# Optimization experiments

Measured on AMD Instinct MI355X. Metric: run time of the kernel, lower is better.

## Reference

```python
import jax, jax.numpy as jnp
import numpy as np

BATCH = 65536
IN_DIM = 512
LATENT = 32
NUM_TRIL = LATENT * (LATENT + 1) // 2  # 528
# torch.tril_indices returns row-major order, same as np.tril_indices
_ROWS, _COLS = np.tril_indices(LATENT)
ROWS = jnp.asarray(_ROWS)
COLS = jnp.asarray(_COLS)
BN_EPS = 1e-5
LRELU_SLOPE = 0.01


def setup_inputs() -> dict:
    key = jax.random.key(0)
    ks = jax.random.split(key, 12)
    x = jax.random.normal(ks[0], (BATCH, IN_DIM), dtype=jnp.float32)
    s_enc = 1.0 / np.sqrt(IN_DIM)
    s_lat = 1.0 / np.sqrt(LATENT)
    return {
        "x": x,
        "W_enc": jax.random.uniform(ks[1], (IN_DIM, LATENT), minval=-s_enc, maxval=s_enc, dtype=jnp.float32),
        "b_enc": jax.random.uniform(ks[2], (LATENT,), minval=-s_enc, maxval=s_enc, dtype=jnp.float32),
        "bn_gamma": jnp.ones((LATENT,), dtype=jnp.float32),
        "bn_beta": jnp.zeros((LATENT,), dtype=jnp.float32),
        "bn_mean": 0.1 * jax.random.normal(ks[3], (LATENT,), dtype=jnp.float32),
        "bn_var": jax.random.uniform(ks[4], (LATENT,), minval=0.5, maxval=1.5, dtype=jnp.float32),
        "W_mu": jax.random.uniform(ks[5], (LATENT, LATENT), minval=-s_lat, maxval=s_lat, dtype=jnp.float32),
        "b_mu": jax.random.uniform(ks[6], (LATENT,), minval=-s_lat, maxval=s_lat, dtype=jnp.float32),
        "W_ch": jax.random.uniform(ks[7], (LATENT, NUM_TRIL), minval=-s_lat, maxval=s_lat, dtype=jnp.float32),
        "b_ch": jax.random.uniform(ks[8], (NUM_TRIL,), minval=-s_lat, maxval=s_lat, dtype=jnp.float32),
    }


def _leaky_relu(v):
    return jnp.where(v >= 0, v, LRELU_SLOPE * v)


def reference(x, W_enc, b_enc, bn_gamma, bn_beta, bn_mean, bn_var, W_mu, b_mu, W_ch, b_ch):
    # downsampled_enc: Linear(512, latent) -> BatchNorm1d (eval mode) -> LeakyReLU
    h = x @ W_enc + b_enc                                        # [B, L]
    h = bn_gamma * (h - bn_mean) * jax.lax.rsqrt(bn_var + BN_EPS) + bn_beta
    h = _leaky_relu(h)
    # mu head
    mus = _leaky_relu(h @ W_mu + b_mu)                           # [B, L]
    # log-cholesky head -> 528 lower-triangular elements
    elts = _leaky_relu(h @ W_ch + b_ch)                          # [B, 528]
    B = x.shape[0]
    L = jnp.zeros((B, LATENT, LATENT), dtype=jnp.float32)
    L = L.at[:, ROWS, COLS].set(elts)                            # scatter into lower triangle
    di = jnp.arange(LATENT)
    diag = L[:, di, di]
    diag = jnp.clip(jax.nn.softplus(diag), 0.001, 100.0) + 0.01
    L = L.at[:, di, di].set(diag)
    # cov = L L^T + 0.01 I
    cov = jnp.einsum('bij,bkj->bik', L, L) + 0.01 * jnp.eye(LATENT, dtype=jnp.float32)
    return (h, mus, cov)
```

## Files before the change

### kernel.cpp

```cpp
#include <hip/hip_runtime.h>
#include <math.h>

constexpr int BATCH  = 65536;
constexpr int IN_DIM = 512;
constexpr int LATENT = 32;
constexpr int NTRIL  = 528;
constexpr float BN_EPS = 1e-5f;
constexpr float SLOPE  = 0.01f;

constexpr int RPB  = 64;
constexpr int SUBR = 16;
constexpr int HSTR = 36;
constexpr int PSTR = 36;

constexpr int LSTRIDE = 584;

__device__ __host__ __forceinline__ constexpr int rstart(int i) {
    const int g = i >> 2, r = i & 3;
    return 4 * (i + 2 * g * (g - 1) + r * g);
}

__device__ __forceinline__ float leaky(float v) {
    return v >= 0.0f ? v : SLOPE * v;
}

extern "C" __global__ __launch_bounds__(256, 4)
void enc_kernel(const float* __restrict__ x,
                const float* __restrict__ W_enc,
                const float* __restrict__ b_enc,
                const float* __restrict__ bn_gamma,
                const float* __restrict__ bn_beta,
                const float* __restrict__ bn_mean,
                const float* __restrict__ bn_var,
                float* __restrict__ h_out)
{
    __shared__ float part[4][RPB][PSTR];

    const int t = threadIdx.x;
    const int w = __builtin_amdgcn_readfirstlane(t >> 6);
    const int l = t & 63;
    const int row0 = blockIdx.x * RPB;

    {
        const float4* __restrict__ xp =
            (const float4*)(x + (size_t)(row0 + l) * IN_DIM + w * (IN_DIM / 4));
        const float* __restrict__ Wq = W_enc + (w * (IN_DIM / 4)) * LATENT;

        float acc[LATENT];
        #pragma unroll
        for (int c = 0; c < LATENT; ++c) acc[c] = 0.0f;

        float4 q0 = xp[0];
        float4 q1 = xp[1];
        #pragma unroll 2
        for (int k4 = 0; k4 < IN_DIM / 16; ++k4) {
            const float4 xv = q0;
            q0 = q1;
            const int pf = (k4 < IN_DIM / 16 - 2) ? (k4 + 2) : (IN_DIM / 16 - 1);
            q1 = xp[pf];

            const float* __restrict__ Wk = Wq + (4 * k4) * LATENT;
            #pragma unroll
            for (int c = 0; c < LATENT; ++c) acc[c] = fmaf(xv.x, Wk[c],            acc[c]);
            #pragma unroll
            for (int c = 0; c < LATENT; ++c) acc[c] = fmaf(xv.y, Wk[LATENT + c],   acc[c]);
            #pragma unroll
            for (int c = 0; c < LATENT; ++c) acc[c] = fmaf(xv.z, Wk[2*LATENT + c], acc[c]);
            #pragma unroll
            for (int c = 0; c < LATENT; ++c) acc[c] = fmaf(xv.w, Wk[3*LATENT + c], acc[c]);
        }

        #pragma unroll
        for (int c4 = 0; c4 < LATENT / 4; ++c4)
            *(float4*)&part[w][l][4 * c4] =
                make_float4(acc[4*c4+0], acc[4*c4+1], acc[4*c4+2], acc[4*c4+3]);
    }
    __syncthreads();

    {
        const int r  = t >> 2;
        const int c0 = (t & 3) * 8;
        float v[8];
        #pragma unroll
        for (int i = 0; i < 8; ++i) v[i] = 0.0f;
        #pragma unroll
        for (int ww = 0; ww < 4; ++ww) {
            const float4 p0 = *(const float4*)&part[ww][r][c0];
            const float4 p1 = *(const float4*)&part[ww][r][c0 + 4];
            v[0]+=p0.x; v[1]+=p0.y; v[2]+=p0.z; v[3]+=p0.w;
            v[4]+=p1.x; v[5]+=p1.y; v[6]+=p1.z; v[7]+=p1.w;
        }
        float hv[8];
        #pragma unroll
        for (int i = 0; i < 8; ++i) {
            const int c = c0 + i;
            float u = v[i] + b_enc[c];
            u = bn_gamma[c] * (u - bn_mean[c]) * rsqrtf(bn_var[c] + BN_EPS) + bn_beta[c];
            hv[i] = leaky(u);
        }
        float4* __restrict__ hp = (float4*)(h_out + (size_t)(row0 + r) * LATENT + c0);
        hp[0] = make_float4(hv[0], hv[1], hv[2], hv[3]);
        hp[1] = make_float4(hv[4], hv[5], hv[6], hv[7]);
    }
}

extern "C" __global__ __launch_bounds__(256)
void dec_kernel(const float* __restrict__ h_in,
                const float* __restrict__ W_mu,
                const float* __restrict__ b_mu,
                const float* __restrict__ W_ch,
                const float* __restrict__ b_ch,
                float* __restrict__ mu_out,
                float* __restrict__ cov_out)
{
    __shared__ float h_sh[RPB][HSTR];
    __shared__ float L_sh[SUBR * LSTRIDE];

    const int t = threadIdx.x;
    const int row0 = blockIdx.x * RPB;

    {
        float4* z4 = (float4*)L_sh;
        const float4 z = make_float4(0.f, 0.f, 0.f, 0.f);
        #pragma unroll 1
        for (int s = t; s < SUBR * LSTRIDE / 4; s += 256) z4[s] = z;
    }

    {
        const int r  = t >> 2;
        const int c0 = (t & 3) * 8;
        const float4* __restrict__ hg =
            (const float4*)(h_in + (size_t)(row0 + r) * LATENT + c0);
        const float4 a0 = hg[0];
        const float4 a1 = hg[1];
        *(float4*)&h_sh[r][c0]     = a0;
        *(float4*)&h_sh[r][c0 + 4] = a1;
    }
    __syncthreads();

    {
        const int c = t & 31;
        const int g = t >> 5;
        float wmu[LATENT];
        #pragma unroll
        for (int k = 0; k < LATENT; ++k) wmu[k] = W_mu[k * LATENT + c];
        const float bm = b_mu[c];
        #pragma unroll
        for (int j = 0; j < 8; ++j) {
            const int r = g * 8 + j;
            const float4* __restrict__ hr = (const float4*)&h_sh[r][0];
            float a = bm;
            #pragma unroll
            for (int k4 = 0; k4 < 8; ++k4) {
                const float4 hvv = hr[k4];
                a += hvv.x*wmu[4*k4+0] + hvv.y*wmu[4*k4+1]
                   + hvv.z*wmu[4*k4+2] + hvv.w*wmu[4*k4+3];
            }
            mu_out[(size_t)(row0 + r) * LATENT + c] = leaky(a);
        }
    }

    #pragma unroll 1
    for (int sb = 0; sb < RPB / SUBR; ++sb) {
        const int rbl = sb * SUBR;

        #pragma unroll 1
        for (int jid = t; jid < 132 * 8; jid += 256) {
            const int q  = jid % 132;
            const int rg = jid / 132;
            const int j0 = 4 * q;
            const int r0s = rbl + rg * 2;

            float4 a0 = make_float4(b_ch[j0+0], b_ch[j0+1], b_ch[j0+2], b_ch[j0+3]);
            float4 a1 = a0;

            const float* __restrict__ wbase = W_ch + j0;
            #pragma unroll
            for (int kq = 0; kq < 8; ++kq) {
                const float4 w0 = *(const float4*)(wbase + (4*kq + 0) * NTRIL);
                const float4 w1 = *(const float4*)(wbase + (4*kq + 1) * NTRIL);
                const float4 w2 = *(const float4*)(wbase + (4*kq + 2) * NTRIL);
                const float4 w3 = *(const float4*)(wbase + (4*kq + 3) * NTRIL);
                const float4 h0 = *(const float4*)&h_sh[r0s    ][4*kq];
                const float4 h1 = *(const float4*)&h_sh[r0s + 1][4*kq];
                a0.x += h0.x*w0.x + h0.y*w1.x + h0.z*w2.x + h0.w*w3.x;
                a0.y += h0.x*w0.y + h0.y*w1.y + h0.z*w2.y + h0.w*w3.y;
                a0.z += h0.x*w0.z + h0.y*w1.z + h0.z*w2.z + h0.w*w3.z;
                a0.w += h0.x*w0.w + h0.y*w1.w + h0.z*w2.w + h0.w*w3.w;
                a1.x += h1.x*w0.x + h1.y*w1.x + h1.z*w2.x + h1.w*w3.x;
                a1.y += h1.x*w0.y + h1.y*w1.y + h1.z*w2.y + h1.w*w3.y;
                a1.z += h1.x*w0.z + h1.y*w1.z + h1.z*w2.z + h1.w*w3.z;
                a1.w += h1.x*w0.w + h1.y*w1.w + h1.z*w2.w + h1.w*w3.w;
            }

            #pragma unroll
            for (int e = 0; e < 4; ++e) {
                const int j = j0 + e;
                int ri = (int)((sqrtf(8.0f * (float)j + 1.0f) - 1.0f) * 0.5f);
                if ((ri + 1) * (ri + 2) / 2 <= j) ++ri;
                if (ri * (ri + 1) / 2 > j) --ri;
                const int ci = j - ri * (ri + 1) / 2;
                const bool isdiag = (ci == ri);
                const int off = rstart(ri) + ci;

                float v0 = (e == 0) ? a0.x : (e == 1) ? a0.y : (e == 2) ? a0.z : a0.w;
                float v1 = (e == 0) ? a1.x : (e == 1) ? a1.y : (e == 2) ? a1.z : a1.w;
                v0 = leaky(v0);
                v1 = leaky(v1);
                if (isdiag) {
                    float s0 = v0 > 20.0f ? v0 : log1pf(__expf(v0));
                    float s1 = v1 > 20.0f ? v1 : log1pf(__expf(v1));
                    v0 = fminf(fmaxf(s0, 0.001f), 100.0f) + 0.01f;
                    v1 = fminf(fmaxf(s1, 0.001f), 100.0f) + 0.01f;
                }
                L_sh[(r0s - rbl) * LSTRIDE + off]       = v0;
                L_sh[(r0s - rbl + 1) * LSTRIDE + off]   = v1;
            }
        }
        __syncthreads();

        {
            const int lr = t >> 4;
            const int p  = t & 15;
            const float* __restrict__ Lb = L_sh + lr * LSTRIDE;

            float a0[16];
            {
                const int s0 = rstart(p);
                #pragma unroll
                for (int qq = 0; qq < 4; ++qq) {
                    const float4 v = *(const float4*)(Lb + s0 + 4*qq);
                    a0[4*qq+0] = (4*qq+0 <= p) ? v.x : 0.0f;
                    a0[4*qq+1] = (4*qq+1 <= p) ? v.y : 0.0f;
                    a0[4*qq+2] = (4*qq+2 <= p) ? v.z : 0.0f;
                    a0[4*qq+3] = (4*qq+3 <= p) ? v.w : 0.0f;
                }
            }
            float a1[32];
            {
                const int i1 = p + 16;
                const int s1 = rstart(i1);
                #pragma unroll
                for (int qq = 0; qq < 8; ++qq) {
                    const float4 v = *(const float4*)(Lb + s1 + 4*qq);
                    a1[4*qq+0] = (4*qq+0 <= i1) ? v.x : 0.0f;
                    a1[4*qq+1] = (4*qq+1 <= i1) ? v.y : 0.0f;
                    a1[4*qq+2] = (4*qq+2 <= i1) ? v.z : 0.0f;
                    a1[4*qq+3] = (4*qq+3 <= i1) ? v.w : 0.0f;
                }
            }

            const size_t grow = (size_t)(row0 + rbl + lr);
            float* __restrict__ cov0 =
                cov_out + grow * (size_t)(LATENT * LATENT) + (size_t)p * LATENT;
            float* __restrict__ cov1 = cov0 + 16 * LATENT;

            float c0[4], c1[4];
            #pragma unroll
            for (int k = 0; k < LATENT; ++k) {
                const int qk = (k >> 2) + 1;
                const float* __restrict__ Lk = Lb + rstart(k);
                float d0 = 0.0f, d1 = 0.0f;
                #pragma unroll
                for (int qq = 0; qq < qk; ++qq) {
                    const float4 w = *(const float4*)(Lk + 4*qq);
                    if (qq < 4) {
                        d0 += a0[4*qq+0]*w.x + a0[4*qq+1]*w.y
                            + a0[4*qq+2]*w.z + a0[4*qq+3]*w.w;
                    }
                    d1 += a1[4*qq+0]*w.x + a1[4*qq+1]*w.y
                        + a1[4*qq+2]*w.z + a1[4*qq+3]*w.w;
                }
                d0 = (k == p)      ? d0 + 0.01f : d0;
                d1 = (k == p + 16) ? d1 + 0.01f : d1;
                c0[k & 3] = d0;
                c1[k & 3] = d1;
                if ((k & 3) == 3) {
                    *(float4*)(cov0 + (k - 3)) = make_float4(c0[0], c0[1], c0[2], c0[3]);
                    *(float4*)(cov1 + (k - 3)) = make_float4(c1[0], c1[1], c1[2], c1[3]);
                }
            }
        }
        __syncthreads();
    }
}

extern "C" void kernel_launch(void* const* d_in, const int* in_sizes, int n_in,
                              void* d_out, int out_size, void* d_ws, size_t ws_size,
                              hipStream_t stream) {
    const float* x        = (const float*)d_in[0];
    const float* W_enc    = (const float*)d_in[1];
    const float* b_enc    = (const float*)d_in[2];
    const float* bn_gamma = (const float*)d_in[3];
    const float* bn_beta  = (const float*)d_in[4];
    const float* bn_mean  = (const float*)d_in[5];
    const float* bn_var   = (const float*)d_in[6];
    const float* W_mu     = (const float*)d_in[7];
    const float* b_mu     = (const float*)d_in[8];
    const float* W_ch     = (const float*)d_in[9];
    const float* b_ch     = (const float*)d_in[10];
    float* out = (float*)d_out;

    float* h_out   = out;
    float* mu_out  = out + (size_t)BATCH * LATENT;
    float* cov_out = out + (size_t)2 * BATCH * LATENT;

    enc_kernel<<<dim3(BATCH / RPB), dim3(256), 0, stream>>>(
        x, W_enc, b_enc, bn_gamma, bn_beta, bn_mean, bn_var, h_out);
    dec_kernel<<<dim3(BATCH / RPB), dim3(256), 0, stream>>>(
        h_out, W_mu, b_mu, W_ch, b_ch, mu_out, cov_out);
}
```

Measured before the change: 672.0 us.

## Split decoder into elements kernel and covariance kernel staging L through output buffer

The fused decoder kernel is split in two. The first kernel computes mu and the 528 Cholesky elements, computing four rows per thread for more weight reuse, and writes them packed into the cov output buffer. A second kernel reloads the packed L from global memory into shared memory, zeroes the padding gaps, and computes L L^T plus 0.01 I, overwriting the same buffer. This removes the large shared-memory footprint and the sub-batch loop with its syncs from the decoder, but adds an extra global write and read of L plus one more kernel launch.

```diff
diff --git a/kernel.cpp b/kernel.cpp
--- a/kernel.cpp
+++ b/kernel.cpp
@@ -9,10 +9,11 @@
 constexpr float SLOPE  = 0.01f;
 
 constexpr int RPB  = 64;
-constexpr int SUBR = 16;
+constexpr int CROWS = 16;
 constexpr int HSTR = 36;
 constexpr int PSTR = 36;
 
+constexpr int LPACK   = 576;
 constexpr int LSTRIDE = 584;
 
 __device__ __host__ __forceinline__ constexpr int rstart(int i) {
@@ -105,26 +106,18 @@
 }
 
 extern "C" __global__ __launch_bounds__(256)
-void dec_kernel(const float* __restrict__ h_in,
-                const float* __restrict__ W_mu,
-                const float* __restrict__ b_mu,
-                const float* __restrict__ W_ch,
-                const float* __restrict__ b_ch,
-                float* __restrict__ mu_out,
-                float* __restrict__ cov_out)
+void elts_kernel(const float* __restrict__ h_in,
+                 const float* __restrict__ W_mu,
+                 const float* __restrict__ b_mu,
+                 const float* __restrict__ W_ch,
+                 const float* __restrict__ b_ch,
+                 float* __restrict__ mu_out,
+                 float* __restrict__ cov_out)
 {
     __shared__ float h_sh[RPB][HSTR];
-    __shared__ float L_sh[SUBR * LSTRIDE];
 
     const int t = threadIdx.x;
     const int row0 = blockIdx.x * RPB;
-
-    {
-        float4* z4 = (float4*)L_sh;
-        const float4 z = make_float4(0.f, 0.f, 0.f, 0.f);
-        #pragma unroll 1
-        for (int s = t; s < SUBR * LSTRIDE / 4; s += 256) z4[s] = z;
-    }
 
     {
         const int r  = t >> 2;
@@ -161,127 +154,188 @@
     }
 
     #pragma unroll 1
-    for (int sb = 0; sb < RPB / SUBR; ++sb) {
-        const int rbl = sb * SUBR;
-
-        #pragma unroll 1
-        for (int jid = t; jid < 132 * 8; jid += 256) {
-            const int q  = jid % 132;
-            const int rg = jid / 132;
-            const int j0 = 4 * q;
-            const int r0s = rbl + rg * 2;
-
-            float4 a0 = make_float4(b_ch[j0+0], b_ch[j0+1], b_ch[j0+2], b_ch[j0+3]);
-            float4 a1 = a0;
-
-            const float* __restrict__ wbase = W_ch + j0;
-            #pragma unroll
-            for (int kq = 0; kq < 8; ++kq) {
-                const float4 w0 = *(const float4*)(wbase + (4*kq + 0) * NTRIL);
-                const float4 w1 = *(const float4*)(wbase + (4*kq + 1) * NTRIL);
-                const float4 w2 = *(const float4*)(wbase + (4*kq + 2) * NTRIL);
-                const float4 w3 = *(const float4*)(wbase + (4*kq + 3) * NTRIL);
-                const float4 h0 = *(const float4*)&h_sh[r0s    ][4*kq];
-                const float4 h1 = *(const float4*)&h_sh[r0s + 1][4*kq];
-                a0.x += h0.x*w0.x + h0.y*w1.x + h0.z*w2.x + h0.w*w3.x;
-                a0.y += h0.x*w0.y + h0.y*w1.y + h0.z*w2.y + h0.w*w3.y;
-                a0.z += h0.x*w0.z + h0.y*w1.z + h0.z*w2.z + h0.w*w3.z;
-                a0.w += h0.x*w0.w + h0.y*w1.w + h0.z*w2.w + h0.w*w3.w;
-                a1.x += h1.x*w0.x + h1.y*w1.x + h1.z*w2.x + h1.w*w3.x;
-                a1.y += h1.x*w0.y + h1.y*w1.y + h1.z*w2.y + h1.w*w3.y;
-                a1.z += h1.x*w0.z + h1.y*w1.z + h1.z*w2.z + h1.w*w3.z;
-                a1.w += h1.x*w0.w + h1.y*w1.w + h1.z*w2.w + h1.w*w3.w;
-            }
-
-            #pragma unroll
-            for (int e = 0; e < 4; ++e) {
-                const int j = j0 + e;
-                int ri = (int)((sqrtf(8.0f * (float)j + 1.0f) - 1.0f) * 0.5f);
-                if ((ri + 1) * (ri + 2) / 2 <= j) ++ri;
-                if (ri * (ri + 1) / 2 > j) --ri;
-                const int ci = j - ri * (ri + 1) / 2;
-                const bool isdiag = (ci == ri);
-                const int off = rstart(ri) + ci;
-
-                float v0 = (e == 0) ? a0.x : (e == 1) ? a0.y : (e == 2) ? a0.z : a0.w;
-                float v1 = (e == 0) ? a1.x : (e == 1) ? a1.y : (e == 2) ? a1.z : a1.w;
-                v0 = leaky(v0);
-                v1 = leaky(v1);
+    for (int jid = t; jid < 132 * 16; jid += 256) {
+        const int q  = jid % 132;
+        const int rg = jid / 132;
+        const int j0 = 4 * q;
+        const int r0s = 4 * rg;
+
+        float4 a0 = make_float4(b_ch[j0+0], b_ch[j0+1], b_ch[j0+2], b_ch[j0+3]);
+        float4 a1 = a0, a2 = a0, a3 = a0;
+
+        const float* __restrict__ wbase = W_ch + j0;
+        #pragma unroll
+        for (int kq = 0; kq < 8; ++kq) {
+            const float4 w0 = *(const float4*)(wbase + (4*kq + 0) * NTRIL);
+            const float4 w1 = *(const float4*)(wbase + (4*kq + 1) * NTRIL);
+            const float4 w2 = *(const float4*)(wbase + (4*kq + 2) * NTRIL);
+            const float4 w3 = *(const float4*)(wbase + (4*kq + 3) * NTRIL);
+            const float4 h0 = *(const float4*)&h_sh[r0s + 0][4*kq];
+            const float4 h1 = *(const float4*)&h_sh[r0s + 1][4*kq];
+            const float4 h2 = *(const float4*)&h_sh[r0s + 2][4*kq];
+            const float4 h3 = *(const float4*)&h_sh[r0s + 3][4*kq];
+            a0.x += h0.x*w0.x + h0.y*w1.x + h0.z*w2.x + h0.w*w3.x;
+            a0.y += h0.x*w0.y + h0.y*w1.y + h0.z*w2.y + h0.w*w3.y;
+            a0.z += h0.x*w0.z + h0.y*w1.z + h0.z*w2.z + h0.w*w3.z;
+            a0.w += h0.x*w0.w + h0.y*w1.w + h0.z*w2.w + h0.w*w3.w;
+            a1.x += h1.x*w0.x + h1.y*w1.x + h1.z*w2.x + h1.w*w3.x;
+            a1.y += h1.x*w0.y + h1.y*w1.y + h1.z*w2.y + h1.w*w3.y;
+            a1.z += h1.x*w0.z + h1.y*w1.z + h1.z*w2.z + h1.w*w3.z;
+            a1.w += h1.x*w0.w + h1.y*w1.w + h1.z*w2.w + h1.w*w3.w;
+            a2.x += h2.x*w0.x + h2.y*w1.x + h2.z*w2.x + h2.w*w3.x;
+            a2.y += h2.x*w0.y + h2.y*w1.y + h2.z*w2.y + h2.w*w3.y;
+            a2.z += h2.x*w0.z + h2.y*w1.z + h2.z*w2.z + h2.w*w3.z;
+            a2.w += h2.x*w0.w + h2.y*w1.w + h2.z*w2.w + h2.w*w3.w;
+            a3.x += h3.x*w0.x + h3.y*w1.x + h3.z*w2.x + h3.w*w3.x;
+            a3.y += h3.x*w0.y + h3.y*w1.y + h3.z*w2.y + h3.w*w3.y;
+            a3.z += h3.x*w0.z + h3.y*w1.z + h3.z*w2.z + h3.w*w3.z;
+            a3.w += h3.x*w0.w + h3.y*w1.w + h3.z*w2.w + h3.w*w3.w;
+        }
+
+        #pragma unroll
+        for (int e = 0; e < 4; ++e) {
+            const int j = j0 + e;
+            int ri = (int)((sqrtf(8.0f * (float)j + 1.0f) - 1.0f) * 0.5f);
+            if ((ri + 1) * (ri + 2) / 2 <= j) ++ri;
+            if (ri * (ri + 1) / 2 > j) --ri;
+            const int ci = j - ri * (ri + 1) / 2;
+            const bool isdiag = (ci == ri);
+            const int off = rstart(ri) + ci;
+
+            #pragma unroll
+            for (int rr = 0; rr < 4; ++rr) {
+                float vv = (rr == 0) ? ((e==0)?a0.x:(e==1)?a0.y:(e==2)?a0.z:a0.w)
+                         : (rr == 1) ? ((e==0)?a1.x:(e==1)?a1.y:(e==2)?a1.z:a1.w)
+                         : (rr == 2) ? ((e==0)?a2.x:(e==1)?a2.y:(e==2)?a2.z:a2.w)
+                                     : ((e==0)?a3.x:(e==1)?a3.y:(e==2)?a3.z:a3.w);
+                vv = leaky(vv);
                 if (isdiag) {
-                    float s0 = v0 > 20.0f ? v0 : log1pf(__expf(v0));
-                    float s1 = v1 > 20.0f ? v1 : log1pf(__expf(v1));
-                    v0 = fminf(fmaxf(s0, 0.001f), 100.0f) + 0.01f;
-                    v1 = fminf(fmaxf(s1, 0.001f), 100.0f) + 0.01f;
+                    float sp = vv > 20.0f ? vv : log1pf(__expf(vv));
+                    vv = fminf(fmaxf(sp, 0.001f), 100.0f) + 0.01f;
                 }
-                L_sh[(r0s - rbl) * LSTRIDE + off]       = v0;
-                L_sh[(r0s - rbl + 1) * LSTRIDE + off]   = v1;
-            }
-        }
-        __syncthreads();
-
+                cov_out[(size_t)(row0 + r0s + rr) * (LATENT * LATENT) + off] = vv;
+            }
+        }
+    }
+}
+
+extern "C" __global__ __launch_bounds__(256)
+void cov_kernel(float* __restrict__ cov_out)
+{
+    __shared__ float L_sh[CROWS * LSTRIDE];
+
+    const int t = threadIdx.x;
+    const int row0b = blockIdx.x * CROWS;
+
+    #pragma unroll 1
+    for (int s = t; s < CROWS * (LPACK / 4); s += 256) {
+        const int lr = s / (LPACK / 4);
+        const int qi = s % (LPACK / 4);
+        const float4 v = *(const float4*)
+            (cov_out + (size_t)(row0b + lr) * (LATENT * LATENT) + 4 * qi);
+        *(float4*)&L_sh[lr * LSTRIDE + 4 * qi] = v;
+    }
+    __syncthreads();
+
+    #pragma unroll 1
+    for (int s = t; s < CROWS * 48; s += 256) {
+        const int lr  = s / 48;
+        const int idx = s % 48;
+        const int g  = idx / 6;
+        const int wv = idx % 6;
+        const int rig = (wv < 3) ? 0 : (wv < 5) ? 1 : 2;
+        const int po  = (wv < 3) ? wv : (wv < 5) ? wv - 3 : 0;
+        const int i   = 4 * g + rig;
+        L_sh[lr * LSTRIDE + rstart(i) + (i + 1) + po] = 0.0f;
+    }
+    __syncthreads();
+
+    {
+        const int lr = t >> 4;
+        const int p  = t & 15;
+        const float* __restrict__ Lb = L_sh + lr * LSTRIDE;
+
+        float li0[16];
         {
-            const int lr = t >> 4;
-            const int p  = t & 15;
-            const float* __restrict__ Lb = L_sh + lr * LSTRIDE;
-
-            float a0[16];
-            {
-                const int s0 = rstart(p);
-                #pragma unroll
-                for (int qq = 0; qq < 4; ++qq) {
-                    const float4 v = *(const float4*)(Lb + s0 + 4*qq);
-                    a0[4*qq+0] = (4*qq+0 <= p) ? v.x : 0.0f;
-                    a0[4*qq+1] = (4*qq+1 <= p) ? v.y : 0.0f;
-                    a0[4*qq+2] = (4*qq+2 <= p) ? v.z : 0.0f;
-                    a0[4*qq+3] = (4*qq+3 <= p) ? v.w : 0.0f;
+            const int s0 = rstart(p);
+            #pragma unroll
+            for (int qq = 0; qq < 4; ++qq) {
+                const float4 v = *(const float4*)(Lb + s0 + 4*qq);
+                li0[4*qq+0] = (4*qq+0 <= p) ? v.x : 0.0f;
+                li0[4*qq+1] = (4*qq+1 <= p) ? v.y : 0.0f;
+                li0[4*qq+2] = (4*qq+2 <= p) ? v.z : 0.0f;
+                li0[4*qq+3] = (4*qq+3 <= p) ? v.w : 0.0f;
+            }
+        }
+        float li1[32];
+        {
+            const int i1 = p + 16;
+            const int s1 = rstart(i1);
+            #pragma unroll
+            for (int qq = 0; qq < 8; ++qq) {
+                const float4 v = *(const float4*)(Lb + s1 + 4*qq);
+                li1[4*qq+0] = (4*qq+0 <= i1) ? v.x : 0.0f;
+                li1[4*qq+1] = (4*qq+1 <= i1) ? v.y : 0.0f;
+                li1[4*qq+2] = (4*qq+2 <= i1) ? v.z : 0.0f;
+                li1[4*qq+3] = (4*qq+3 <= i1) ? v.w : 0.0f;
+            }
+        }
+
+        float* __restrict__ cov0 =
+            cov_out + (size_t)(row0b + lr) * (LATENT * LATENT) + (size_t)p * LATENT;
+        float* __restrict__ cov1 = cov0 + 16 * LATENT;
+
+        float cr0[16], cr1[16];
+
+        #pragma unroll
+        for (int k = 0; k < 16; ++k) {
+            const int qk = (k >> 2) + 1;
+            const float* __restrict__ Lk = Lb + rstart(k);
+            float d0 = 0.0f, d1 = 0.0f;
+            #pragma unroll
+            for (int qq = 0; qq < qk; ++qq) {
+                const float4 wv = *(const float4*)(Lk + 4*qq);
+                d0 += li0[4*qq+0]*wv.x + li0[4*qq+1]*wv.y
+                    + li0[4*qq+2]*wv.z + li0[4*qq+3]*wv.w;
+                d1 += li1[4*qq+0]*wv.x + li1[4*qq+1]*wv.y
+                    + li1[4*qq+2]*wv.z + li1[4*qq+3]*wv.w;
+            }
+            cr0[k] = (k == p) ? d0 + 0.01f : d0;
+            cr1[k] = d1;
+        }
+        #pragma unroll
+        for (int k4 = 0; k4 < 4; ++k4) {
+            *(float4*)(cov0 + 4*k4) = make_float4(cr0[4*k4], cr0[4*k4+1], cr0[4*k4+2], cr0[4*k4+3]);
+            *(float4*)(cov1 + 4*k4) = make_float4(cr1[4*k4], cr1[4*k4+1], cr1[4*k4+2], cr1[4*k4+3]);
+        }
+
+        #pragma unroll
+        for (int k = 16; k < 32; ++k) {
+            const int qk = (k >> 2) + 1;
+            const float* __restrict__ Lk = Lb + rstart(k);
+            float d0 = 0.0f, d1 = 0.0f;
+            #pragma unroll
+            for (int qq = 0; qq < 4; ++qq) {
+                const float4 wv = *(const float4*)(Lk + 4*qq);
+                d0 += li0[4*qq+0]*wv.x + li0[4*qq+1]*wv.y
+                    + li0[4*qq+2]*wv.z + li0[4*qq+3]*wv.w;
+            }
+            #pragma unroll
+            for (int qq = 0; qq < 8; ++qq) {
+                if (qq < qk) {
+                    const float4 wv = *(const float4*)(Lk + 4*qq);
+                    d1 += li1[4*qq+0]*wv.x + li1[4*qq+1]*wv.y
+                        + li1[4*qq+2]*wv.z + li1[4*qq+3]*wv.w;
                 }
             }
-            float a1[32];
-            {
-                const int i1 = p + 16;
-                const int s1 = rstart(i1);
-                #pragma unroll
-                for (int qq = 0; qq < 8; ++qq) {
-                    const float4 v = *(const float4*)(Lb + s1 + 4*qq);
-                    a1[4*qq+0] = (4*qq+0 <= i1) ? v.x : 0.0f;
-                    a1[4*qq+1] = (4*qq+1 <= i1) ? v.y : 0.0f;
-                    a1[4*qq+2] = (4*qq+2 <= i1) ? v.z : 0.0f;
-                    a1[4*qq+3] = (4*qq+3 <= i1) ? v.w : 0.0f;
-                }
-            }
-
-            const size_t grow = (size_t)(row0 + rbl + lr);
-            float* __restrict__ cov0 =
-                cov_out + grow * (size_t)(LATENT * LATENT) + (size_t)p * LATENT;
-            float* __restrict__ cov1 = cov0 + 16 * LATENT;
-
-            float c0[4], c1[4];
-            #pragma unroll
-            for (int k = 0; k < LATENT; ++k) {
-                const int qk = (k >> 2) + 1;
-                const float* __restrict__ Lk = Lb + rstart(k);
-                float d0 = 0.0f, d1 = 0.0f;
-                #pragma unroll
-                for (int qq = 0; qq < qk; ++qq) {
-                    const float4 w = *(const float4*)(Lk + 4*qq);
-                    if (qq < 4) {
-                        d0 += a0[4*qq+0]*w.x + a0[4*qq+1]*w.y
-                            + a0[4*qq+2]*w.z + a0[4*qq+3]*w.w;
-                    }
-                    d1 += a1[4*qq+0]*w.x + a1[4*qq+1]*w.y
-                        + a1[4*qq+2]*w.z + a1[4*qq+3]*w.w;
-                }
-                d0 = (k == p)      ? d0 + 0.01f : d0;
-                d1 = (k == p + 16) ? d1 + 0.01f : d1;
-                c0[k & 3] = d0;
-                c1[k & 3] = d1;
-                if ((k & 3) == 3) {
-                    *(float4*)(cov0 + (k - 3)) = make_float4(c0[0], c0[1], c0[2], c0[3]);
-                    *(float4*)(cov1 + (k - 3)) = make_float4(c1[0], c1[1], c1[2], c1[3]);
-                }
-            }
-        }
-        __syncthreads();
+            cr0[k-16] = d0;
+            cr1[k-16] = (k == p + 16) ? d1 + 0.01f : d1;
+        }
+        #pragma unroll
+        for (int k4 = 0; k4 < 4; ++k4) {
+            *(float4*)(cov0 + 16 + 4*k4) = make_float4(cr0[4*k4], cr0[4*k4+1], cr0[4*k4+2], cr0[4*k4+3]);
+            *(float4*)(cov1 + 16 + 4*k4) = make_float4(cr1[4*k4], cr1[4*k4+1], cr1[4*k4+2], cr1[4*k4+3]);
+        }
     }
 }
 
@@ -307,6 +361,7 @@
 
     enc_kernel<<<dim3(BATCH / RPB), dim3(256), 0, stream>>>(
         x, W_enc, b_enc, bn_gamma, bn_beta, bn_mean, bn_var, h_out);
-    dec_kernel<<<dim3(BATCH / RPB), dim3(256), 0, stream>>>(
+    elts_kernel<<<dim3(BATCH / RPB), dim3(256), 0, stream>>>(
         h_out, W_mu, b_mu, W_ch, b_ch, mu_out, cov_out);
-}
+    cov_kernel<<<dim3(BATCH / CROWS), dim3(256), 0, stream>>>(cov_out);
+}
```

New measurement: 807.1 us. +20.1%, slower.
